# Performance work log

Measured on AMD Instinct MI355X. Metric: run time of the kernel, lower is better.

The kernel has to match this reference:

```python
import jax, jax.numpy as jnp
import numpy as np

NEG_INF = -1e9
LRELU_SLOPE = 0.2  # torch GAT default leaky_relu negative slope


def setup_inputs() -> dict:
    key = jax.random.key(0)
    k1, k2, k3, k4, k5 = jax.random.split(key, 5)
    N, F_IN, H, DH = 4096, 1433, 8, 8  # n_nodes, in_features, n_heads, per-head dim (n_hidden=64)
    vert = jax.random.normal(k1, (N, F_IN), dtype=jnp.float32)
    edge = jax.random.randint(k2, (N, N), 0, 2, dtype=jnp.int32)  # dense adjacency mask
    W = jax.random.normal(k3, (F_IN, H * DH), dtype=jnp.float32) * 0.05
    a_l = jax.random.normal(k4, (H, DH), dtype=jnp.float32) * 0.05
    a_r = jax.random.normal(k5, (H, DH), dtype=jnp.float32) * 0.05
    return {"vert": vert, "edge": edge, "W": W, "a_l": a_l, "a_r": a_r}


def reference(vert, edge, W, a_l, a_r):
    # GAT-style edge-affinity layer (is_concat=True) + ELU; dropout is identity (eval mode).
    N = vert.shape[0]
    H, DH = a_l.shape
    g = (vert @ W).reshape(N, H, DH)                      # [N,H,Dh] projected node features
    sl = jnp.einsum('nhd,hd->nh', g, a_l)                 # source-node attention term
    sr = jnp.einsum('nhd,hd->nh', g, a_r)                 # target-node attention term
    e = sl[:, None, :] + sr[None, :, :]                   # [N,N,H]: attn([g_i || g_j])
    e = jnp.where(e >= 0, e, LRELU_SLOPE * e)             # leaky_relu
    mask = (edge != 0)[:, :, None]                        # [N,N,1]
    e = jnp.where(mask, e, NEG_INF)                       # mask non-edges
    a = jax.nn.softmax(e, axis=1)                         # normalize over neighbors j
    out = jnp.einsum('ijh,jhd->ihd', a, g).reshape(N, H * DH)  # aggregate + concat heads
    return jax.nn.elu(out)
```

## Files before the change

### kernel.cpp

```cpp
#include <hip/hip_runtime.h>
#include <hip/hip_bf16.h>

#define NN 4096
#define FIN 1433
#define NH 8
#define DH 8
#define HD 64
#define KP 1472
#define LOG2E 1.44269504f
#define NJS 4
#define NCHK ((NN / NJS) / 128)

typedef unsigned int u32;
typedef unsigned long long u64;
typedef float v4f __attribute__((ext_vector_type(4)));
typedef _Float16 f16;
typedef _Float16 h2 __attribute__((ext_vector_type(2)));
typedef _Float16 f16x8 __attribute__((ext_vector_type(8)));

static __device__ __forceinline__ short f2h16(float f) {
    union { f16 h; short s; } u; u.h = (f16)f; return u.s;
}
static __device__ __forceinline__ h2 u2h2(u32 x) {
    union { u32 u; h2 h; } v; v.u = x; return v.h;
}
static __device__ __forceinline__ u32 h22u(h2 x) {
    union { h2 h; u32 u; } v; v.h = x; return v.u;
}

#if __has_builtin(__builtin_amdgcn_sbfe)
#define SBFE1(x, k) __builtin_amdgcn_sbfe((int)(x), (k), 1)
#else
#define SBFE1(x, k) (((int)((x) << (31 - (k)))) >> 31)
#endif

__global__ __launch_bounds__(256) void k_wprep(const float* __restrict__ W,
                                               short* __restrict__ Wt) {
    __shared__ float Ts[64][65];
    const int c = blockIdx.x;
    const int u = threadIdx.x;
    const int n4 = (u & 15) * 4;
    const int kr = u >> 4;
#pragma unroll
    for (int q = 0; q < 4; ++q) {
        const int kl = kr + q * 16;
        const int kg = c * 64 + kl;
        v4f v = {0.f, 0.f, 0.f, 0.f};
        if (kg < FIN) v = *(const v4f*)&W[(size_t)kg * HD + n4];
        *(v4f*)&Ts[kl][n4] = v;
    }
    __syncthreads();
    const int n = u >> 2;
    const int koff = (u & 3) * 16;
    __align__(16) short tmp[16];
#pragma unroll
    for (int r = 0; r < 16; ++r) tmp[r] = f2h16(Ts[koff + r][n]);
    *(uint4*)&Wt[(size_t)n * KP + c * 64 + koff]     = *(uint4*)&tmp[0];
    *(uint4*)&Wt[(size_t)n * KP + c * 64 + koff + 8] = *(uint4*)&tmp[8];
}

__global__ __launch_bounds__(256, 4) void k_gemm(
    const float* __restrict__ vert, const short* __restrict__ Wt,
    const float* __restrict__ al, const float* __restrict__ ar,
    short* __restrict__ gT, short* __restrict__ eB, short* __restrict__ eD,
    float* __restrict__ Rw)
{
    __shared__ float cacc[4][16][64];

    const int t = threadIdx.x, lane = t & 63, w = t >> 6;
    const int ml = lane & 15, q = lane >> 4;
    const int i0 = blockIdx.x * 16;
    const float* vrow = vert + (size_t)(i0 + ml) * FIN;

    v4f acc[4];
#pragma unroll
    for (int g = 0; g < 4; ++g) acc[g] = (v4f){0.f, 0.f, 0.f, 0.f};

    for (int c = w; c < 45; c += 4) {
        const int k0 = c * 32 + q * 8;
        v4f a0, a1;
        if (k0 + 7 < FIN) {
            a0 = *(const v4f*)&vrow[k0];
            a1 = *(const v4f*)&vrow[k0 + 4];
        } else {
            float tmp[8];
#pragma unroll
            for (int e = 0; e < 8; ++e)
                tmp[e] = (k0 + e < FIN) ? vrow[k0 + e] : 0.f;
            a0 = (v4f){tmp[0], tmp[1], tmp[2], tmp[3]};
            a1 = (v4f){tmp[4], tmp[5], tmp[6], tmp[7]};
        }
        const f16x8 af = {(f16)a0.x, (f16)a0.y, (f16)a0.z, (f16)a0.w,
                          (f16)a1.x, (f16)a1.y, (f16)a1.z, (f16)a1.w};
#pragma unroll
        for (int g = 0; g < 4; ++g) {
            const f16x8 bf = *(const f16x8*)&Wt[(size_t)(g * 16 + ml) * KP + k0];
            acc[g] = __builtin_amdgcn_mfma_f32_16x16x32_f16(af, bf, acc[g], 0, 0, 0);
        }
    }

#pragma unroll
    for (int g = 0; g < 4; ++g)
#pragma unroll
        for (int r = 0; r < 4; ++r)
            cacc[w][q * 4 + r][g * 16 + ml] = acc[g][r];
    __syncthreads();

    const int m = t >> 4, n4 = (t & 15) * 4;
    v4f s = (v4f){0.f, 0.f, 0.f, 0.f};
#pragma unroll
    for (int ww = 0; ww < 4; ++ww) s += *(const v4f*)&cacc[ww][m][n4];

#pragma unroll
    for (int e = 0; e < 4; ++e)
        gT[(size_t)(n4 + e) * NN + i0 + m] = f2h16(s[e]);

    float pl = s.x * al[n4] + s.y * al[n4 + 1] + s.z * al[n4 + 2] + s.w * al[n4 + 3];
    float pr = s.x * ar[n4] + s.y * ar[n4 + 1] + s.z * ar[n4 + 2] + s.w * ar[n4 + 3];
    pl += __shfl_xor(pl, 1, 64);
    pr += __shfl_xor(pr, 1, 64);
    if ((t & 1) == 0) {
        const int h = (t & 15) >> 1;
        const int node = i0 + m;
        eB[h * NN + node] = f2h16(exp2f(pr * LOG2E));
        eD[h * NN + node] = f2h16(exp2f(0.2f * pr * LOG2E));
        Rw[node * NH + h] = exp2f(-0.8f * pl * LOG2E);
    }
}

__global__ __launch_bounds__(256, 4) void k_attn(
    const int* __restrict__ edge, const short* __restrict__ gT,
    const short* __restrict__ eB, const short* __restrict__ eD,
    const float* __restrict__ Rw,
    float* __restrict__ numw, float* __restrict__ denw)
{
    __shared__ __align__(16) short Gt[2][65][136];
    __shared__ __align__(16) short sB[2][8][136];
    __shared__ __align__(16) short sD[2][8][136];
    __shared__ u32 mA[2][16][4];
    __shared__ u32 mB[2][16][4];

    const int t = threadIdx.x, lane = t & 63, w = t >> 6;
    const int ml = lane & 15, quad = lane >> 4;
    const int i0 = blockIdx.x * 16;
    const int js = blockIdx.y;
    const int jbase = js * (NN / NJS);
    const int h0 = w, h1 = w + 4;

    h2 Ri[2];
    {
        const f16 r0 = (f16)Rw[(i0 + ml) * NH + h0];
        const f16 r1 = (f16)Rw[(i0 + ml) * NH + h1];
        Ri[0] = (h2){r0, r0};
        Ri[1] = (h2){r1, r1};
    }

    if (t < 136) { Gt[0][64][t] = 0x3C00; Gt[1][64][t] = 0x3C00; }

    const int grow = t >> 3, gseg = (t & 7) * 16;
    const int bh = (t >> 3) & 7, bseg = (t & 7) * 16;
    const int erow = w * 4;

    {
        const int j0 = jbase;
        *(uint4*)&Gt[0][grow][gseg]          = *(const uint4*)&gT[grow * NN + j0 + gseg];
        *(uint4*)&Gt[0][grow][gseg + 8]      = *(const uint4*)&gT[grow * NN + j0 + gseg + 8];
        *(uint4*)&Gt[0][grow + 32][gseg]     = *(const uint4*)&gT[(grow + 32) * NN + j0 + gseg];
        *(uint4*)&Gt[0][grow + 32][gseg + 8] = *(const uint4*)&gT[(grow + 32) * NN + j0 + gseg + 8];
        if (t < 64) {
            *(uint4*)&sB[0][bh][bseg]     = *(const uint4*)&eB[bh * NN + j0 + bseg];
            *(uint4*)&sB[0][bh][bseg + 8] = *(const uint4*)&eB[bh * NN + j0 + bseg + 8];
        } else if (t < 128) {
            *(uint4*)&sD[0][bh][bseg]     = *(const uint4*)&eD[bh * NN + j0 + bseg];
            *(uint4*)&sD[0][bh][bseg + 8] = *(const uint4*)&eD[bh * NN + j0 + bseg + 8];
        }
#pragma unroll
        for (int rr = 0; rr < 4; ++rr) {
            const int row = erow + rr;
            const int2 e2 = *(const int2*)&edge[(i0 + row) * NN + j0 + 2 * lane];
            const u64 bA = __ballot(e2.x != 0);
            const u64 bB = __ballot(e2.y != 0);
            if (lane == 0)  { mA[0][row][0] = (u32)bA;         mB[0][row][0] = (u32)bB; }
            if (lane == 32) { mA[0][row][1] = (u32)(bA >> 32); mB[0][row][1] = (u32)(bB >> 32); }
        }
    }
    __syncthreads();

    v4f acc[2];
    acc[0] = (v4f){0.f, 0.f, 0.f, 0.f};
    acc[1] = (v4f){0.f, 0.f, 0.f, 0.f};

    const int qb4 = quad * 4;
    const int brow0 = (ml < 8) ? (h0 * 8 + ml) : 64;
    const int brow1 = (ml < 8) ? (h1 * 8 + ml) : 64;

    for (int c = 0; c < NCHK; ++c) {
        const int cb = c & 1, nb = cb ^ 1;
        const bool pf = (c + 1) < NCHK;
        uint4 pg[4], pbd0, pbd1; int2 pe[4];
        if (pf) {
            const int j0 = jbase + (c + 1) * 128;
            pg[0] = *(const uint4*)&gT[grow * NN + j0 + gseg];
            pg[1] = *(const uint4*)&gT[grow * NN + j0 + gseg + 8];
            pg[2] = *(const uint4*)&gT[(grow + 32) * NN + j0 + gseg];
            pg[3] = *(const uint4*)&gT[(grow + 32) * NN + j0 + gseg + 8];
            if (t < 64) {
                pbd0 = *(const uint4*)&eB[bh * NN + j0 + bseg];
                pbd1 = *(const uint4*)&eB[bh * NN + j0 + bseg + 8];
            } else if (t < 128) {
                pbd0 = *(const uint4*)&eD[bh * NN + j0 + bseg];
                pbd1 = *(const uint4*)&eD[bh * NN + j0 + bseg + 8];
            }
#pragma unroll
            for (int rr = 0; rr < 4; ++rr)
                pe[rr] = *(const int2*)&edge[(i0 + erow + rr) * NN + j0 + 2 * lane];
        }
        const uint2 wa = *(const uint2*)&mA[cb][ml][0];
        const uint2 wb = *(const uint2*)&mB[cb][ml][0];
#pragma unroll
        for (int s = 0; s < 4; ++s) {
            const uint4 bu0 = *(const uint4*)&sB[cb][h0][s * 32 + quad * 8];
            const uint4 du0 = *(const uint4*)&sD[cb][h0][s * 32 + quad * 8];
            const uint4 bu1 = *(const uint4*)&sB[cb][h1][s * 32 + quad * 8];
            const uint4 du1 = *(const uint4*)&sD[cb][h1][s * 32 + quad * 8];
            const uint4 gu0 = *(const uint4*)&Gt[cb][brow0][s * 32 + quad * 8];
            const uint4 gu1 = *(const uint4*)&Gt[cb][brow1][s * 32 + quad * 8];
            const int base = ((s & 1) << 4) + qb4;
            const u32 WA = ((s >> 1) ? wa.y : wa.x) >> base;
            const u32 WB = ((s >> 1) ? wb.y : wb.x) >> base;
            u32 m[4];
#pragma unroll
            for (int k = 0; k < 4; ++k) {
                const int ea = SBFE1(WA, k);
                const int eb = SBFE1(WB, k);
                m[k] = __builtin_amdgcn_perm((u32)eb, (u32)ea, 0x05040100u);
            }
            u32 aw0[4], aw1[4];
#pragma unroll
            for (int k = 0; k < 4; ++k) {
                const u32 rd0 = h22u(Ri[0] * u2h2((&du0.x)[k]));
                const u32 rd1 = h22u(Ri[1] * u2h2((&du1.x)[k]));
                u32 p0, p1;
                asm("v_pk_max_f16 %0, %1, %2" : "=v"(p0) : "v"(rd0), "v"((&bu0.x)[k]));
                asm("v_pk_max_f16 %0, %1, %2" : "=v"(p1) : "v"(rd1), "v"((&bu1.x)[k]));
                aw0[k] = p0 & m[k];
                aw1[k] = p1 & m[k];
            }
            union { uint4 u; f16x8 h; } a0u, a1u, g0u, g1u;
            a0u.u = (uint4){aw0[0], aw0[1], aw0[2], aw0[3]};
            a1u.u = (uint4){aw1[0], aw1[1], aw1[2], aw1[3]};
            g0u.u = gu0; g1u.u = gu1;
            acc[0] = __builtin_amdgcn_mfma_f32_16x16x32_f16(a0u.h, g0u.h, acc[0], 0, 0, 0);
            acc[1] = __builtin_amdgcn_mfma_f32_16x16x32_f16(a1u.h, g1u.h, acc[1], 0, 0, 0);
        }
        if (pf) {
            *(uint4*)&Gt[nb][grow][gseg]          = pg[0];
            *(uint4*)&Gt[nb][grow][gseg + 8]      = pg[1];
            *(uint4*)&Gt[nb][grow + 32][gseg]     = pg[2];
            *(uint4*)&Gt[nb][grow + 32][gseg + 8] = pg[3];
            if (t < 64) {
                *(uint4*)&sB[nb][bh][bseg]     = pbd0;
                *(uint4*)&sB[nb][bh][bseg + 8] = pbd1;
            } else if (t < 128) {
                *(uint4*)&sD[nb][bh][bseg]     = pbd0;
                *(uint4*)&sD[nb][bh][bseg + 8] = pbd1;
            }
#pragma unroll
            for (int rr = 0; rr < 4; ++rr) {
                const int row = erow + rr;
                const u64 bA = __ballot(pe[rr].x != 0);
                const u64 bB = __ballot(pe[rr].y != 0);
                if (lane == 0)  { mA[nb][row][0] = (u32)bA;         mB[nb][row][0] = (u32)bB; }
                if (lane == 32) { mA[nb][row][1] = (u32)(bA >> 32); mB[nb][row][1] = (u32)(bB >> 32); }
            }
        }
        __syncthreads();
    }

    float* nw = numw + (size_t)js * NN * HD;
    float* dw = denw + (size_t)js * NN * NH;
    const int ibase = i0 + quad * 4;
#pragma unroll
    for (int hh = 0; hh < 2; ++hh) {
        const int h = w + hh * 4;
#pragma unroll
        for (int r = 0; r < 4; ++r) {
            if (ml < 8)       nw[(ibase + r) * HD + h * 8 + ml] = acc[hh][r];
            else if (ml == 8) dw[(ibase + r) * NH + h]          = acc[hh][r];
        }
    }
}

__global__ __launch_bounds__(256) void k_comb(
    const float* __restrict__ numw, const float* __restrict__ denw,
    float* __restrict__ out)
{
    const int gid = blockIdx.x * 256 + threadIdx.x;
    const int i = gid >> 6, h = (gid & 63) >> 3;
    float num = 0.f, den = 0.f;
#pragma unroll
    for (int s = 0; s < NJS; ++s) {
        num += numw[s * NN * HD + gid];
        den += denw[s * NN * NH + i * NH + h];
    }
    float x = num / den;
    out[gid] = (x > 0.f) ? x : (__expf(x) - 1.f);
}

extern "C" void kernel_launch(void* const* d_in, const int* in_sizes, int n_in,
                              void* d_out, int out_size, void* d_ws, size_t ws_size,
                              hipStream_t stream) {
    const float* vert = (const float*)d_in[0];
    const int*   edge = (const int*)d_in[1];
    const float* W    = (const float*)d_in[2];
    const float* al   = (const float*)d_in[3];
    const float* ar   = (const float*)d_in[4];
    float* out = (float*)d_out;

    char* ws = (char*)d_ws;
    short* gT   = (short*)ws;
    short* eB   = (short*)(ws + 512 * 1024);
    short* eD   = (short*)(ws + 576 * 1024);
    float* Rw   = (float*)(ws + 640 * 1024);
    short* Wt   = (short*)(ws + 768 * 1024);
    float* numw = (float*)(ws + 1024 * 1024);
    float* denw = (float*)(ws + 5 * 1024 * 1024);

    hipLaunchKernelGGL(k_wprep, dim3(23), dim3(256), 0, stream, W, Wt);
    hipLaunchKernelGGL(k_gemm, dim3(NN / 16), dim3(256), 0, stream,
                       vert, Wt, al, ar, gT, eB, eD, Rw);
    hipLaunchKernelGGL(k_attn, dim3(NN / 16, NJS), dim3(256), 0, stream,
                       edge, gT, eB, eD, Rw, numw, denw);
    hipLaunchKernelGGL(k_comb, dim3(NN * HD / 256), dim3(256), 0, stream,
                       numw, denw, out);
}
```

Before: 150.4 us.

## Precompute edge bitmask, drop LDS staging in attention, atomically reduce splits

Adds a prep kernel that packs the int32 adjacency into a bitmask and zeroes the num/den accumulators. The attention kernel then reads the bitmask and the gT/eB/eD operands straight from global memory, with no LDS double-buffering or barriers. It doubles the j-splits and merges partial results with atomicAdd instead of per-split workspace buffers. The GEMM kernel moves to 512 threads with 8 waves sharing the K loop. This trades the in-kernel ballot work and the large partial buffers for an extra launch, repeated global/L2 reads of the operands, and atomics. The packed mask bit order is changed to match (even and odd columns interleaved).

After: 197.2 us. +31.1%, slower.

```diff
diff --git a/kernel.cpp b/kernel.cpp
--- a/kernel.cpp
+++ b/kernel.cpp
@@ -8,7 +8,7 @@
 #define HD 64
 #define KP 1472
 #define LOG2E 1.44269504f
-#define NJS 4
+#define NJS 8
 #define NCHK ((NN / NJS) / 128)
 
 typedef unsigned int u32;
@@ -33,6 +33,22 @@
 #else
 #define SBFE1(x, k) (((int)((x) << (31 - (k)))) >> 31)
 #endif
+
+__global__ __launch_bounds__(256) void k_eprep(const int* __restrict__ edge,
+                                               u64* __restrict__ emask,
+                                               float* __restrict__ zbuf) {
+    const int t = threadIdx.x, lane = t & 63, w = t >> 6;
+    const int row = blockIdx.x;
+    const int* erow = edge + (size_t)row * NN + w * 1024;
+    u64* mrow = emask + (size_t)row * (NN / 64) + w * 16;
+#pragma unroll
+    for (int it = 0; it < 16; ++it) {
+        const int e = erow[it * 64 + lane];
+        const u64 b = __ballot(e != 0);
+        if (lane == 0) mrow[it] = b;
+    }
+    if (t < 72) zbuf[row * 72 + t] = 0.f;
+}
 
 __global__ __launch_bounds__(256) void k_wprep(const float* __restrict__ W,
                                                short* __restrict__ Wt) {
@@ -59,13 +75,13 @@
     *(uint4*)&Wt[(size_t)n * KP + c * 64 + koff + 8] = *(uint4*)&tmp[8];
 }
 
-__global__ __launch_bounds__(256, 4) void k_gemm(
+__global__ __launch_bounds__(512, 2) void k_gemm(
     const float* __restrict__ vert, const short* __restrict__ Wt,
     const float* __restrict__ al, const float* __restrict__ ar,
     short* __restrict__ gT, short* __restrict__ eB, short* __restrict__ eD,
     float* __restrict__ Rw)
 {
-    __shared__ float cacc[4][16][64];
+    __shared__ float cacc[8][16][68];
 
     const int t = threadIdx.x, lane = t & 63, w = t >> 6;
     const int ml = lane & 15, q = lane >> 4;
@@ -76,7 +92,7 @@
 #pragma unroll
     for (int g = 0; g < 4; ++g) acc[g] = (v4f){0.f, 0.f, 0.f, 0.f};
 
-    for (int c = w; c < 45; c += 4) {
+    for (int c = w; c < 45; c += 8) {
         const int k0 = c * 32 + q * 8;
         v4f a0, a1;
         if (k0 + 7 < FIN) {
@@ -106,46 +122,45 @@
             cacc[w][q * 4 + r][g * 16 + ml] = acc[g][r];
     __syncthreads();
 
-    const int m = t >> 4, n4 = (t & 15) * 4;
-    v4f s = (v4f){0.f, 0.f, 0.f, 0.f};
-#pragma unroll
-    for (int ww = 0; ww < 4; ++ww) s += *(const v4f*)&cacc[ww][m][n4];
-
-#pragma unroll
-    for (int e = 0; e < 4; ++e)
-        gT[(size_t)(n4 + e) * NN + i0 + m] = f2h16(s[e]);
-
-    float pl = s.x * al[n4] + s.y * al[n4 + 1] + s.z * al[n4 + 2] + s.w * al[n4 + 3];
-    float pr = s.x * ar[n4] + s.y * ar[n4 + 1] + s.z * ar[n4 + 2] + s.w * ar[n4 + 3];
-    pl += __shfl_xor(pl, 1, 64);
-    pr += __shfl_xor(pr, 1, 64);
-    if ((t & 1) == 0) {
-        const int h = (t & 15) >> 1;
-        const int node = i0 + m;
-        eB[h * NN + node] = f2h16(exp2f(pr * LOG2E));
-        eD[h * NN + node] = f2h16(exp2f(0.2f * pr * LOG2E));
-        Rw[node * NH + h] = exp2f(-0.8f * pl * LOG2E);
+    if (t < 256) {
+        const int m = t >> 4, n4 = (t & 15) * 4;
+        v4f s = (v4f){0.f, 0.f, 0.f, 0.f};
+#pragma unroll
+        for (int ww = 0; ww < 8; ++ww) s += *(const v4f*)&cacc[ww][m][n4];
+
+#pragma unroll
+        for (int e = 0; e < 4; ++e)
+            gT[(size_t)(n4 + e) * NN + i0 + m] = f2h16(s[e]);
+
+        float pl = s.x * al[n4] + s.y * al[n4 + 1] + s.z * al[n4 + 2] + s.w * al[n4 + 3];
+        float pr = s.x * ar[n4] + s.y * ar[n4 + 1] + s.z * ar[n4 + 2] + s.w * ar[n4 + 3];
+        pl += __shfl_xor(pl, 1, 64);
+        pr += __shfl_xor(pr, 1, 64);
+        if ((t & 1) == 0) {
+            const int h = (t & 15) >> 1;
+            const int node = i0 + m;
+            eB[h * NN + node] = f2h16(exp2f(pr * LOG2E));
+            eD[h * NN + node] = f2h16(exp2f(0.2f * pr * LOG2E));
+            Rw[node * NH + h] = exp2f(-0.8f * pl * LOG2E);
+        }
     }
 }
 
 __global__ __launch_bounds__(256, 4) void k_attn(
-    const int* __restrict__ edge, const short* __restrict__ gT,
+    const uint4* __restrict__ emask, const short* __restrict__ gT,
     const short* __restrict__ eB, const short* __restrict__ eD,
     const float* __restrict__ Rw,
-    float* __restrict__ numw, float* __restrict__ denw)
+    float* __restrict__ num, float* __restrict__ den)
 {
-    __shared__ __align__(16) short Gt[2][65][136];
-    __shared__ __align__(16) short sB[2][8][136];
-    __shared__ __align__(16) short sD[2][8][136];
-    __shared__ u32 mA[2][16][4];
-    __shared__ u32 mB[2][16][4];
-
     const int t = threadIdx.x, lane = t & 63, w = t >> 6;
     const int ml = lane & 15, quad = lane >> 4;
     const int i0 = blockIdx.x * 16;
-    const int js = blockIdx.y;
-    const int jbase = js * (NN / NJS);
+    const int jbase = blockIdx.y * (NN / NJS);
     const int h0 = w, h1 = w + 4;
+    const bool mhi = (ml >= 8);
+    const u32 one2 = 0x3C003C00u;
+    const uint4 ones4 = (uint4){one2, one2, one2, one2};
+    const int qsh = quad * 8;
 
     h2 Ri[2];
     {
@@ -155,84 +170,37 @@
         Ri[1] = (h2){r1, r1};
     }
 
-    if (t < 136) { Gt[0][64][t] = 0x3C00; Gt[1][64][t] = 0x3C00; }
-
-    const int grow = t >> 3, gseg = (t & 7) * 16;
-    const int bh = (t >> 3) & 7, bseg = (t & 7) * 16;
-    const int erow = w * 4;
-
-    {
-        const int j0 = jbase;
-        *(uint4*)&Gt[0][grow][gseg]          = *(const uint4*)&gT[grow * NN + j0 + gseg];
-        *(uint4*)&Gt[0][grow][gseg + 8]      = *(const uint4*)&gT[grow * NN + j0 + gseg + 8];
-        *(uint4*)&Gt[0][grow + 32][gseg]     = *(const uint4*)&gT[(grow + 32) * NN + j0 + gseg];
-        *(uint4*)&Gt[0][grow + 32][gseg + 8] = *(const uint4*)&gT[(grow + 32) * NN + j0 + gseg + 8];
-        if (t < 64) {
-            *(uint4*)&sB[0][bh][bseg]     = *(const uint4*)&eB[bh * NN + j0 + bseg];
-            *(uint4*)&sB[0][bh][bseg + 8] = *(const uint4*)&eB[bh * NN + j0 + bseg + 8];
-        } else if (t < 128) {
-            *(uint4*)&sD[0][bh][bseg]     = *(const uint4*)&eD[bh * NN + j0 + bseg];
-            *(uint4*)&sD[0][bh][bseg + 8] = *(const uint4*)&eD[bh * NN + j0 + bseg + 8];
-        }
-#pragma unroll
-        for (int rr = 0; rr < 4; ++rr) {
-            const int row = erow + rr;
-            const int2 e2 = *(const int2*)&edge[(i0 + row) * NN + j0 + 2 * lane];
-            const u64 bA = __ballot(e2.x != 0);
-            const u64 bB = __ballot(e2.y != 0);
-            if (lane == 0)  { mA[0][row][0] = (u32)bA;         mB[0][row][0] = (u32)bB; }
-            if (lane == 32) { mA[0][row][1] = (u32)(bA >> 32); mB[0][row][1] = (u32)(bB >> 32); }
-        }
-    }
-    __syncthreads();
+    const uint4* mrow = emask + (size_t)(i0 + ml) * (NN / 128) + (jbase >> 7);
+    const short* gp0 = gT + (size_t)(h0 * 8 + (ml & 7)) * NN;
+    const short* gp1 = gT + (size_t)(h1 * 8 + (ml & 7)) * NN;
+    const short* bp0 = eB + (size_t)h0 * NN;
+    const short* dp0 = eD + (size_t)h0 * NN;
+    const short* bp1 = eB + (size_t)h1 * NN;
+    const short* dp1 = eD + (size_t)h1 * NN;
 
     v4f acc[2];
     acc[0] = (v4f){0.f, 0.f, 0.f, 0.f};
     acc[1] = (v4f){0.f, 0.f, 0.f, 0.f};
 
-    const int qb4 = quad * 4;
-    const int brow0 = (ml < 8) ? (h0 * 8 + ml) : 64;
-    const int brow1 = (ml < 8) ? (h1 * 8 + ml) : 64;
-
     for (int c = 0; c < NCHK; ++c) {
-        const int cb = c & 1, nb = cb ^ 1;
-        const bool pf = (c + 1) < NCHK;
-        uint4 pg[4], pbd0, pbd1; int2 pe[4];
-        if (pf) {
-            const int j0 = jbase + (c + 1) * 128;
-            pg[0] = *(const uint4*)&gT[grow * NN + j0 + gseg];
-            pg[1] = *(const uint4*)&gT[grow * NN + j0 + gseg + 8];
-            pg[2] = *(const uint4*)&gT[(grow + 32) * NN + j0 + gseg];
-            pg[3] = *(const uint4*)&gT[(grow + 32) * NN + j0 + gseg + 8];
-            if (t < 64) {
-                pbd0 = *(const uint4*)&eB[bh * NN + j0 + bseg];
-                pbd1 = *(const uint4*)&eB[bh * NN + j0 + bseg + 8];
-            } else if (t < 128) {
-                pbd0 = *(const uint4*)&eD[bh * NN + j0 + bseg];
-                pbd1 = *(const uint4*)&eD[bh * NN + j0 + bseg + 8];
-            }
-#pragma unroll
-            for (int rr = 0; rr < 4; ++rr)
-                pe[rr] = *(const int2*)&edge[(i0 + erow + rr) * NN + j0 + 2 * lane];
-        }
-        const uint2 wa = *(const uint2*)&mA[cb][ml][0];
-        const uint2 wb = *(const uint2*)&mB[cb][ml][0];
+        const uint4 mw = mrow[c];
+        const int jc = jbase + c * 128 + qsh;
 #pragma unroll
         for (int s = 0; s < 4; ++s) {
-            const uint4 bu0 = *(const uint4*)&sB[cb][h0][s * 32 + quad * 8];
-            const uint4 du0 = *(const uint4*)&sD[cb][h0][s * 32 + quad * 8];
-            const uint4 bu1 = *(const uint4*)&sB[cb][h1][s * 32 + quad * 8];
-            const uint4 du1 = *(const uint4*)&sD[cb][h1][s * 32 + quad * 8];
-            const uint4 gu0 = *(const uint4*)&Gt[cb][brow0][s * 32 + quad * 8];
-            const uint4 gu1 = *(const uint4*)&Gt[cb][brow1][s * 32 + quad * 8];
-            const int base = ((s & 1) << 4) + qb4;
-            const u32 WA = ((s >> 1) ? wa.y : wa.x) >> base;
-            const u32 WB = ((s >> 1) ? wb.y : wb.x) >> base;
+            const int j0 = jc + s * 32;
+            const uint4 bu0 = *(const uint4*)&bp0[j0];
+            const uint4 du0 = *(const uint4*)&dp0[j0];
+            const uint4 bu1 = *(const uint4*)&bp1[j0];
+            const uint4 du1 = *(const uint4*)&dp1[j0];
+            const uint4 gu0 = *(const uint4*)&gp0[j0];
+            const uint4 gu1 = *(const uint4*)&gp1[j0];
+
+            const u32 w8 = (&mw.x)[s] >> qsh;
             u32 m[4];
 #pragma unroll
             for (int k = 0; k < 4; ++k) {
-                const int ea = SBFE1(WA, k);
-                const int eb = SBFE1(WB, k);
+                const int ea = SBFE1(w8, 2 * k);
+                const int eb = SBFE1(w8, 2 * k + 1);
                 m[k] = __builtin_amdgcn_perm((u32)eb, (u32)ea, 0x05040100u);
             }
             u32 aw0[4], aw1[4];
@@ -249,61 +217,34 @@
             union { uint4 u; f16x8 h; } a0u, a1u, g0u, g1u;
             a0u.u = (uint4){aw0[0], aw0[1], aw0[2], aw0[3]};
             a1u.u = (uint4){aw1[0], aw1[1], aw1[2], aw1[3]};
-            g0u.u = gu0; g1u.u = gu1;
+            g0u.u = mhi ? ones4 : gu0;
+            g1u.u = mhi ? ones4 : gu1;
             acc[0] = __builtin_amdgcn_mfma_f32_16x16x32_f16(a0u.h, g0u.h, acc[0], 0, 0, 0);
             acc[1] = __builtin_amdgcn_mfma_f32_16x16x32_f16(a1u.h, g1u.h, acc[1], 0, 0, 0);
         }
-        if (pf) {
-            *(uint4*)&Gt[nb][grow][gseg]          = pg[0];
-            *(uint4*)&Gt[nb][grow][gseg + 8]      = pg[1];
-            *(uint4*)&Gt[nb][grow + 32][gseg]     = pg[2];
-            *(uint4*)&Gt[nb][grow + 32][gseg + 8] = pg[3];
-            if (t < 64) {
-                *(uint4*)&sB[nb][bh][bseg]     = pbd0;
-                *(uint4*)&sB[nb][bh][bseg + 8] = pbd1;
-            } else if (t < 128) {
-                *(uint4*)&sD[nb][bh][bseg]     = pbd0;
-                *(uint4*)&sD[nb][bh][bseg + 8] = pbd1;
-            }
-#pragma unroll
-            for (int rr = 0; rr < 4; ++rr) {
-                const int row = erow + rr;
-                const u64 bA = __ballot(pe[rr].x != 0);
-                const u64 bB = __ballot(pe[rr].y != 0);
-                if (lane == 0)  { mA[nb][row][0] = (u32)bA;         mB[nb][row][0] = (u32)bB; }
-                if (lane == 32) { mA[nb][row][1] = (u32)(bA >> 32); mB[nb][row][1] = (u32)(bB >> 32); }
-            }
-        }
-        __syncthreads();
-    }
-
-    float* nw = numw + (size_t)js * NN * HD;
-    float* dw = denw + (size_t)js * NN * NH;
+    }
+
     const int ibase = i0 + quad * 4;
 #pragma unroll
     for (int hh = 0; hh < 2; ++hh) {
         const int h = w + hh * 4;
 #pragma unroll
         for (int r = 0; r < 4; ++r) {
-            if (ml < 8)       nw[(ibase + r) * HD + h * 8 + ml] = acc[hh][r];
-            else if (ml == 8) dw[(ibase + r) * NH + h]          = acc[hh][r];
+            if (ml < 8)
+                atomicAdd(&num[(size_t)(ibase + r) * HD + h * 8 + ml], acc[hh][r]);
+            else if (ml == 8)
+                atomicAdd(&den[(size_t)(ibase + r) * NH + h], acc[hh][r]);
         }
     }
 }
 
 __global__ __launch_bounds__(256) void k_comb(
-    const float* __restrict__ numw, const float* __restrict__ denw,
+    const float* __restrict__ num, const float* __restrict__ den,
     float* __restrict__ out)
 {
     const int gid = blockIdx.x * 256 + threadIdx.x;
     const int i = gid >> 6, h = (gid & 63) >> 3;
-    float num = 0.f, den = 0.f;
-#pragma unroll
-    for (int s = 0; s < NJS; ++s) {
-        num += numw[s * NN * HD + gid];
-        den += denw[s * NN * NH + i * NH + h];
-    }
-    float x = num / den;
+    const float x = num[gid] / den[i * NH + h];
     out[gid] = (x > 0.f) ? x : (__expf(x) - 1.f);
 }
 
@@ -318,19 +259,21 @@
     float* out = (float*)d_out;
 
     char* ws = (char*)d_ws;
-    short* gT   = (short*)ws;
-    short* eB   = (short*)(ws + 512 * 1024);
-    short* eD   = (short*)(ws + 576 * 1024);
-    float* Rw   = (float*)(ws + 640 * 1024);
-    short* Wt   = (short*)(ws + 768 * 1024);
-    float* numw = (float*)(ws + 1024 * 1024);
-    float* denw = (float*)(ws + 5 * 1024 * 1024);
-
+    short* gT    = (short*)ws;
+    short* eB    = (short*)(ws + 512 * 1024);
+    short* eD    = (short*)(ws + 576 * 1024);
+    float* Rw    = (float*)(ws + 640 * 1024);
+    short* Wt    = (short*)(ws + 768 * 1024);
+    u64*   emask = (u64*)(ws + 1024 * 1024);
+    float* num   = (float*)(ws + 3 * 1024 * 1024);
+    float* den   = (float*)(ws + 4 * 1024 * 1024);
+
+    hipLaunchKernelGGL(k_eprep, dim3(NN), dim3(256), 0, stream, edge, emask, num);
     hipLaunchKernelGGL(k_wprep, dim3(23), dim3(256), 0, stream, W, Wt);
-    hipLaunchKernelGGL(k_gemm, dim3(NN / 16), dim3(256), 0, stream,
+    hipLaunchKernelGGL(k_gemm, dim3(NN / 16), dim3(512), 0, stream,
                        vert, Wt, al, ar, gT, eB, eD, Rw);
     hipLaunchKernelGGL(k_attn, dim3(NN / 16, NJS), dim3(256), 0, stream,
-                       edge, gT, eB, eD, Rw, numw, denw);
+                       (const uint4*)emask, gT, eB, eD, Rw, num, den);
     hipLaunchKernelGGL(k_comb, dim3(NN * HD / 256), dim3(256), 0, stream,
-                       numw, denw, out);
-}
+                       num, den, out);
+}
```
